# Performance work log

Measured on AMD Instinct MI355X. Metric: run time of the kernel, lower is better.

The kernel has to match this reference:

```python
import jax, jax.numpy as jnp
import numpy as np

D_MODEL = 1024
H = 16
D_K = D_MODEL // H  # 64
B, S = 2, 2048


def setup_inputs() -> dict:
    key = jax.random.key(0)
    ks = jax.random.split(key, 8)
    scale = 1.0 / np.sqrt(D_MODEL)
    return {
        "q": jax.random.normal(ks[0], (B, S, D_MODEL), dtype=jnp.float32),
        "k": jax.random.normal(ks[1], (B, S, D_MODEL), dtype=jnp.float32),
        "v": jax.random.normal(ks[2], (B, S, D_MODEL), dtype=jnp.float32),
        "W_q": jax.random.normal(ks[3], (H, D_MODEL, D_K), dtype=jnp.float32) * scale,
        "W_k": jax.random.normal(ks[4], (H, D_MODEL, D_K), dtype=jnp.float32) * scale,
        "W_v": jax.random.normal(ks[5], (H, D_MODEL, D_K), dtype=jnp.float32) * scale,
        "W_o": jax.random.normal(ks[6], (D_MODEL, H * D_K), dtype=jnp.float32) * scale,
        "b_o": jnp.zeros((D_MODEL,), dtype=jnp.float32),
    }


def reference(q, k, v, W_q, W_k, W_v, W_o, b_o):
    b, s, _ = q.shape
    h, _, d_k = W_q.shape
    inv_sqrt_dk = jnp.asarray(1.0 / np.sqrt(d_k), q.dtype)
    # per-head projections: [b, h, s, d_k]
    qh = jnp.einsum("bsd,hdk->bhsk", q, W_q)
    kh = jnp.einsum("bsd,hdk->bhsk", k, W_k)
    vh = jnp.einsum("bsd,hdk->bhsk", v, W_v)
    # scaled dot product attention
    scores = jnp.einsum("bhqk,bhsk->bhqs", qh, kh) * inv_sqrt_dk  # [b,h,S,S]
    attn = jax.nn.softmax(scores, axis=-1)
    ctx = jnp.einsum("bhqs,bhsk->bhqk", attn, vh)  # [b,h,S,d_k]
    # chunk over heads + concat along feature dim -> [b, S, h*d_k], head-major
    ctx = ctx.transpose(0, 2, 1, 3).reshape(b, s, h * d_k)
    # final linear
    return ctx @ W_o.T + b_o
```

## Files before the change

### kernel.cpp

```cpp
#include <hip/hip_runtime.h>
#include <cstdint>
#include <cstddef>


typedef unsigned short bf16_t;
typedef __attribute__((ext_vector_type(8))) short short8;
typedef __attribute__((ext_vector_type(4))) float f32x4;

__device__ __forceinline__ uint32_t fbits(float f) {
  union { float f; uint32_t u; } v; v.f = f; return v.u;
}
__device__ __forceinline__ bf16_t f2bf(float f) {
  uint32_t u = fbits(f);
  return (bf16_t)((u + 0x7FFFu + ((u >> 16) & 1u)) >> 16);
}
__device__ __forceinline__ uint32_t packbf2(float lo, float hi) {
  uint32_t a = fbits(hi) + 0x8000u;
  uint32_t b = fbits(lo) + 0x8000u;
  return __builtin_amdgcn_perm(a, b, 0x07060302u);
}
__device__ __forceinline__ int4 cvt8(f32x4 lo, f32x4 hi) {
  return make_int4((int)packbf2(lo.x, lo.y), (int)packbf2(lo.z, lo.w),
                   (int)packbf2(hi.x, hi.y), (int)packbf2(hi.z, hi.w));
}

__device__ __forceinline__ void gload16(const bf16_t* g, bf16_t* l) {
  __builtin_amdgcn_global_load_lds(
      (const __attribute__((address_space(1))) void*)g,
      (__attribute__((address_space(3))) void*)l, 16, 0, 0);
}

__global__ void prep_kernel(const float* __restrict__ Wo,
                            const float* __restrict__ Wq, const float* __restrict__ Wk,
                            const float* __restrict__ Wv,
                            const float* __restrict__ q, const float* __restrict__ k,
                            const float* __restrict__ v,
                            bf16_t* __restrict__ Woo,
                            bf16_t* __restrict__ Wtq, bf16_t* __restrict__ Wtk,
                            bf16_t* __restrict__ Wtv,
                            bf16_t* __restrict__ qb, bf16_t* __restrict__ kb,
                            bf16_t* __restrict__ vb) {
  int blk = blockIdx.x;
  int tid = threadIdx.x;
  if (blk < 1024) {
    int i = blk * 256 + tid;
    f32x4 val = ((const f32x4*)Wo)[i];
    ushort4 o;
    o.x = f2bf(val.x); o.y = f2bf(val.y); o.z = f2bf(val.z); o.w = f2bf(val.w);
    ((ushort4*)Woo)[i] = o;
  } else if (blk < 2560) {
    int blk2 = blk - 1024;
    int z = blk2 >> 9, t = blk2 & 511;
    const float* W = z == 0 ? Wq : z == 1 ? Wk : Wv;
    bf16_t* Wt = z == 0 ? Wtq : z == 1 ? Wtk : Wtv;
    int h = t >> 5, d0 = (t & 31) * 32;
    __shared__ float tile[32][65];
    const float* src = W + ((size_t)h << 16) + (size_t)d0 * 64;
    int d = tid >> 3;
#pragma unroll
    for (int j = 0; j < 2; j++) {
      int dk = (tid & 7) * 8 + j * 4;
      *(f32x4*)&tile[d][dk] = *(const f32x4*)(src + d * 64 + dk);
    }
    __syncthreads();
    int dk2 = tid >> 2, c = tid & 3;
    union { ushort s[8]; int4 v; } o;
#pragma unroll
    for (int j = 0; j < 8; j++) o.s[j] = f2bf(tile[c * 8 + j][dk2]);
    *(int4*)(Wt + (size_t)(h * 64 + dk2) * 1024 + d0 + c * 8) = o.v;
  } else {
    int blk3 = blk - 2560;
    int z = blk3 >> 11;
    int t3 = blk3 & 2047;
    const float* src = z == 0 ? q : z == 1 ? k : v;
    bf16_t* dst = z == 0 ? qb : z == 1 ? kb : vb;
    int i = t3 * 256 + tid;
    f32x4 lo = ((const f32x4*)src)[i * 2];
    f32x4 hi = ((const f32x4*)src)[i * 2 + 1];
    ((int4*)dst)[i] = cvt8(lo, hi);
  }
}

__global__ __launch_bounds__(256) void gemm_proj_kernel(
    const bf16_t* __restrict__ A0, const bf16_t* __restrict__ A1, const bf16_t* __restrict__ A2,
    const bf16_t* __restrict__ B0, const bf16_t* __restrict__ B1, const bf16_t* __restrict__ B2,
    bf16_t* __restrict__ O0, bf16_t* __restrict__ O1, bf16_t* __restrict__ O2,
    float s0)
{
  const int bid = blockIdx.x;
  const int nIdx = bid / 96;
  const int g = bid - nIdx * 96;
  const int z = g % 3;
  const int m0 = (g / 3) * 128, n0 = nIdx * 128;

  const bf16_t* A  = z == 0 ? A0 : z == 1 ? A1 : A2;
  const bf16_t* Bt = z == 0 ? B0 : z == 1 ? B1 : B2;
  bf16_t* Cout     = z == 0 ? O0 : z == 1 ? O1 : O2;
  const float scale = z == 0 ? s0 : 1.0f;
  const int K = 1024;

  __shared__ alignas(16) bf16_t smem[18432];

  const int tid = threadIdx.x;
  const int lane = tid & 63, wave = tid >> 6;
  const int wm = wave >> 1, wn = wave & 1;
  const int quad = lane >> 4, l15 = lane & 15;

  f32x4 acc[4][4];
#pragma unroll
  for (int i = 0; i < 4; i++)
#pragma unroll
    for (int j = 0; j < 4; j++) acc[i][j] = (f32x4)0.0f;

  const int srow = tid >> 2, scol = (tid & 3) * 8;
  const bf16_t* pa0 = A  + (size_t)(m0 + srow) * K + scol;
  const bf16_t* pa1 = pa0 + (size_t)64 * K;
  const bf16_t* pb0 = Bt + (size_t)(n0 + srow) * K + scol;
  const bf16_t* pb1 = pb0 + (size_t)64 * K;
  const int lws = wave * 512;

  gload16(pa0, smem + lws);
  gload16(pa1, smem + 2048 + lws);
  gload16(pb0, smem + 4096 + lws);
  gload16(pb1, smem + 6144 + lws);
  __syncthreads();

  for (int it = 0; it < 32; ++it) {
    const int cur = (it & 1) * 8192;
    if (it < 31) {
      const int nxt = ((it + 1) & 1) * 8192;
      const int ko = (it + 1) * 32;
      gload16(pa0 + ko, smem + nxt + lws);
      gload16(pa1 + ko, smem + nxt + 2048 + lws);
      gload16(pb0 + ko, smem + nxt + 4096 + lws);
      gload16(pb1 + ko, smem + nxt + 6144 + lws);
    }

    short8 af[4], bfr[4];
#pragma unroll
    for (int mi = 0; mi < 4; mi++)
      af[mi] = *(const short8*)(smem + cur + (wm * 64 + mi * 16 + l15) * 32 + quad * 8);
#pragma unroll
    for (int ni = 0; ni < 4; ni++)
      bfr[ni] = *(const short8*)(smem + cur + 4096 + (wn * 64 + ni * 16 + l15) * 32 + quad * 8);
#pragma unroll
    for (int mi = 0; mi < 4; mi++)
#pragma unroll
      for (int ni = 0; ni < 4; ni++)
        acc[mi][ni] = __builtin_amdgcn_mfma_f32_16x16x32_bf16(af[mi], bfr[ni], acc[mi][ni], 0, 0, 0);

    __syncthreads();
  }

  const int s0r = m0 & 2047, bb = m0 >> 11, hp = n0 >> 6;
  if (z < 2) {
    bf16_t* slot = smem + wn * 9216;
#pragma unroll
    for (int ni = 0; ni < 4; ni++)
#pragma unroll
      for (int mi = 0; mi < 4; mi++)
#pragma unroll
        for (int r = 0; r < 4; r++)
          slot[(wm * 64 + mi * 16 + quad * 4 + r) * 72 + ni * 16 + l15] =
              f2bf(acc[mi][ni][r] * scale);
    __syncthreads();
#pragma unroll
    for (int rd = 0; rd < 8; ++rd) {
      int idx = rd * 256 + tid;
      int si = idx >> 10, mm = (idx >> 3) & 127, c8 = idx & 7;
      int4 val = *(const int4*)(smem + si * 9216 + mm * 72 + c8 * 8);
      *(int4*)(Cout + ((size_t)((bb * 16 + hp + si) * 2048 + s0r + mm)) * 64 + c8 * 8) = val;
    }
  } else {
    bf16_t* slot = smem + wn * 8704;
#pragma unroll
    for (int ni = 0; ni < 4; ni++)
#pragma unroll
      for (int mi = 0; mi < 4; mi++) {
        uint2 pk = make_uint2(packbf2(acc[mi][ni][0], acc[mi][ni][1]),
                              packbf2(acc[mi][ni][2], acc[mi][ni][3]));
        *(uint2*)(slot + (ni * 16 + l15) * 136 + wm * 64 + mi * 16 + quad * 4) = pk;
      }
    __syncthreads();
#pragma unroll
    for (int rd = 0; rd < 8; ++rd) {
      int idx = rd * 256 + tid;
      int si = idx >> 10, c = (idx >> 4) & 63, ck = idx & 15;
      int4 val = *(const int4*)(smem + si * 8704 + c * 136 + ck * 8);
      *(int4*)(Cout + (size_t)(bb * 16 + hp + si) * 131072 + (size_t)c * 2048 + s0r + ck * 8) = val;
    }
  }
}

__global__ __launch_bounds__(256) void gemm_out_kernel(
    const bf16_t* __restrict__ A, const bf16_t* __restrict__ Bt,
    float* __restrict__ C, const float* __restrict__ bias)
{
  const int K = 1024, N = 1024;
  __shared__ alignas(16) bf16_t smem[12288];
  const int tid = threadIdx.x;
  const int lane = tid & 63, wave = tid >> 6;
  const int quad = lane >> 4, l15 = lane & 15;
  const int m0 = (blockIdx.x & 31) * 128, n0 = (blockIdx.x >> 5) * 64;

  f32x4 acc[2][4];
#pragma unroll
  for (int i = 0; i < 2; i++)
#pragma unroll
    for (int j = 0; j < 4; j++) acc[i][j] = (f32x4)0.0f;

  const int srow = tid >> 2, scol = (tid & 3) * 8;
  const bf16_t* pa0 = A  + (size_t)(m0 + srow) * K + scol;
  const bf16_t* pa1 = pa0 + (size_t)64 * K;
  const bf16_t* pb  = Bt + (size_t)(n0 + srow) * K + scol;
  const int lws = wave * 512;

  gload16(pa0, smem + lws);
  gload16(pa1, smem + 2048 + lws);
  gload16(pb,  smem + 4096 + lws);
  __syncthreads();

  for (int it = 0; it < 32; ++it) {
    const int cur = (it & 1) * 6144;
    if (it < 31) {
      const int nxt = ((it + 1) & 1) * 6144;
      const int ko = (it + 1) * 32;
      gload16(pa0 + ko, smem + nxt + lws);
      gload16(pa1 + ko, smem + nxt + 2048 + lws);
      gload16(pb + ko,  smem + nxt + 4096 + lws);
    }

    short8 af[2], bfr[4];
#pragma unroll
    for (int mi = 0; mi < 2; mi++)
      af[mi] = *(const short8*)(smem + cur + (wave * 32 + mi * 16 + l15) * 32 + quad * 8);
#pragma unroll
    for (int ni = 0; ni < 4; ni++)
      bfr[ni] = *(const short8*)(smem + cur + 4096 + (ni * 16 + l15) * 32 + quad * 8);
#pragma unroll
    for (int mi = 0; mi < 2; mi++)
#pragma unroll
      for (int ni = 0; ni < 4; ni++)
        acc[mi][ni] = __builtin_amdgcn_mfma_f32_16x16x32_bf16(af[mi], bfr[ni], acc[mi][ni], 0, 0, 0);

    __syncthreads();
  }

#pragma unroll
  for (int ni = 0; ni < 4; ni++) {
    int col = n0 + ni * 16 + l15;
    float bv = bias[col];
#pragma unroll
    for (int mi = 0; mi < 2; mi++) {
      int row = m0 + wave * 32 + mi * 16 + quad * 4;
#pragma unroll
      for (int r = 0; r < 4; r++)
        C[(size_t)(row + r) * N + col] = acc[mi][ni][r] + bv;
    }
  }
}

__global__ __launch_bounds__(256) void flash_kernel(
    const bf16_t* __restrict__ qh, const bf16_t* __restrict__ kh,
    const bf16_t* __restrict__ vT, bf16_t* __restrict__ ctx)
{
  __shared__ alignas(16) bf16_t KtF[2][4096];
  __shared__ alignas(16) bf16_t VtF[2][4096];
  __shared__ alignas(16) bf16_t PtF[8192];
  const int tid = threadIdx.x, lane = tid & 63, wave = tid >> 6;
  const int quad = lane >> 4, l15 = lane & 15;
  const int gid = blockIdx.x;
  const int hb = gid & 31;
  const int h = hb & 15, b = hb >> 4;
  const int q0 = (gid >> 5) * 128;
  const size_t headoff = (size_t)hb * 2048 * 64;
  const bf16_t* Q = qh + headoff;
  const bf16_t* K = kh + headoff;
  const bf16_t* V = vT + headoff;

  short8 qf[2][2];
#pragma unroll
  for (int g = 0; g < 2; g++)
#pragma unroll
    for (int ks = 0; ks < 2; ks++)
      qf[g][ks] = *(const short8*)(Q + (size_t)(q0 + wave * 32 + g * 16 + l15) * 64
                                   + ks * 32 + quad * 8);

  f32x4 O[2][4];
#pragma unroll
  for (int g = 0; g < 2; g++)
#pragma unroll
    for (int mi = 0; mi < 4; mi++) O[g][mi] = (f32x4)0.0f;
  f32x4 lacc[2] = {(f32x4)0.0f, (f32x4)0.0f};

  const bf16_t* Kp = K + (size_t)((wave >> 1) * 16 + l15) * 64 + (wave & 1) * 32 + quad * 8;
  const bf16_t* Vp = V + (size_t)((wave >> 1) * 16 + l15) * 2048 + (wave & 1) * 32 + quad * 8;
  const int lws = wave * 512;
  const int pwb = wave * 4096 + ((quad >> 1) * 16 + l15) * 16 + 8 * (quad & 1);

  auto stage = [&](int buf, int t) {
    gload16(Kp + (size_t)t * 4096,        &KtF[buf][lws]);
    gload16(Kp + (size_t)t * 4096 + 2048, &KtF[buf][lws + 2048]);
    gload16(Vp + (size_t)t * 64,          &VtF[buf][lws]);
    gload16(Vp + (size_t)t * 64 + 65536,  &VtF[buf][lws + 2048]);
  };

  auto body = [&](int buf) {
    f32x4 S[2][4];
#pragma unroll
    for (int g = 0; g < 2; g++)
#pragma unroll
      for (int mi = 0; mi < 4; mi++) S[g][mi] = (f32x4)0.0f;
    __builtin_amdgcn_s_setprio(1);
#pragma unroll
    for (int ks = 0; ks < 2; ks++) {
#pragma unroll
      for (int mi = 0; mi < 4; mi++) {
        short8 kf = *(const short8*)(&KtF[buf][(mi * 2 + ks) * 512 + lane * 8]);
        S[0][mi] = __builtin_amdgcn_mfma_f32_16x16x32_bf16(kf, qf[0][ks], S[0][mi], 0, 0, 0);
        S[1][mi] = __builtin_amdgcn_mfma_f32_16x16x32_bf16(kf, qf[1][ks], S[1][mi], 0, 0, 0);
      }
    }
    __builtin_amdgcn_s_setprio(0);
#pragma unroll
    for (int g = 0; g < 2; g++) {
#pragma unroll
      for (int mi = 0; mi < 4; mi++)
#pragma unroll
        for (int r = 0; r < 4; r++)
          S[g][mi][r] = __builtin_amdgcn_exp2f(S[g][mi][r]);
      lacc[g] += (S[g][0] + S[g][1]) + (S[g][2] + S[g][3]);
    }
#pragma unroll
    for (int g = 0; g < 2; g++)
#pragma unroll
      for (int mi = 0; mi < 4; mi++) {
        uint2 pk = make_uint2(packbf2(S[g][mi][0], S[g][mi][1]),
                              packbf2(S[g][mi][2], S[g][mi][3]));
        *(uint2*)((char*)PtF + pwb + g * 2048 + (mi >> 1) * 1024 + (mi & 1) * 512) = pk;
      }
    __builtin_amdgcn_s_setprio(1);
#pragma unroll
    for (int ks = 0; ks < 2; ks++) {
      short8 pf0 = *(const short8*)(&PtF[wave * 2048 + (ks * 64 + lane) * 8]);
      short8 pf1 = *(const short8*)(&PtF[wave * 2048 + 1024 + (ks * 64 + lane) * 8]);
#pragma unroll
      for (int mi = 0; mi < 4; mi++) {
        short8 vf = *(const short8*)(&VtF[buf][(mi * 2 + ks) * 512 + lane * 8]);
        O[0][mi] = __builtin_amdgcn_mfma_f32_16x16x32_bf16(vf, pf0, O[0][mi], 0, 0, 0);
        O[1][mi] = __builtin_amdgcn_mfma_f32_16x16x32_bf16(vf, pf1, O[1][mi], 0, 0, 0);
      }
    }
    __builtin_amdgcn_s_setprio(0);
  };

  stage(0, 0);
  __syncthreads();
  for (int it = 0; it < 32; ++it) {
    if (it < 31) stage((it + 1) & 1, it + 1);
    body(it & 1);
    __syncthreads();
  }

#pragma unroll
  for (int g = 0; g < 2; g++) {
    float l = (lacc[g][0] + lacc[g][1]) + (lacc[g][2] + lacc[g][3]);
    l += __shfl_xor(l, 16, 64);
    l += __shfl_xor(l, 32, 64);
    float inv = 1.0f / l;
    int qrow = q0 + wave * 32 + g * 16 + l15;
    bf16_t* crow = ctx + ((size_t)(b * 2048 + qrow)) * 1024 + h * 64;
#pragma unroll
    for (int mi = 0; mi < 4; mi++) {
      uint2 pk = make_uint2(packbf2(O[g][mi][0] * inv, O[g][mi][1] * inv),
                            packbf2(O[g][mi][2] * inv, O[g][mi][3] * inv));
      *(uint2*)(crow + mi * 16 + quad * 4) = pk;
    }
  }
}

extern "C" void kernel_launch(void* const* d_in, const int* in_sizes, int n_in,
                              void* d_out, int out_size, void* d_ws, size_t ws_size,
                              hipStream_t stream)
{
  const float* q  = (const float*)d_in[0];
  const float* k  = (const float*)d_in[1];
  const float* v  = (const float*)d_in[2];
  const float* Wq = (const float*)d_in[3];
  const float* Wk = (const float*)d_in[4];
  const float* Wv = (const float*)d_in[5];
  const float* Wo = (const float*)d_in[6];
  const float* bo = (const float*)d_in[7];
  float* out = (float*)d_out;

  const size_t NX = (size_t)4096 * 1024;
  const size_t NW = (size_t)1024 * 1024;

  char* p = (char*)d_ws;
  bf16_t* Wtq = (bf16_t*)p; p += NW * 2;
  bf16_t* Wtk = (bf16_t*)p; p += NW * 2;
  bf16_t* Wtv = (bf16_t*)p; p += NW * 2;
  bf16_t* Wob = (bf16_t*)p; p += NW * 2;
  bf16_t* qb  = (bf16_t*)p; p += NX * 2;
  bf16_t* kb  = (bf16_t*)p; p += NX * 2;
  bf16_t* vb  = (bf16_t*)p; p += NX * 2;
  bf16_t* qhb = (bf16_t*)p; p += NX * 2;
  bf16_t* khb = (bf16_t*)p; p += NX * 2;
  bf16_t* vTb = (bf16_t*)p; p += NX * 2;
  bf16_t* ctxb = (bf16_t*)p; p += NX * 2;

  prep_kernel<<<8704, 256, 0, stream>>>(Wo, Wq, Wk, Wv, q, k, v,
                                        Wob, Wtq, Wtk, Wtv, qb, kb, vb);

  const float qscale = 0.125f * 1.44269504088896340736f;
  gemm_proj_kernel<<<768, 256, 0, stream>>>(qb, kb, vb, Wtq, Wtk, Wtv,
                                            qhb, khb, vTb, qscale);

  flash_kernel<<<512, 256, 0, stream>>>(qhb, khb, vTb, ctxb);

  gemm_out_kernel<<<512, 256, 0, stream>>>(ctxb, Wob, out, bo);

  (void)in_sizes; (void)n_in; (void)out_size; (void)ws_size;
}
```

Measured before the change: 217.6 us.

## Use 512-thread flash blocks with register-staged K/V double buffering

Doubles the flash-attention block to 8 waves covering 256 query rows, so each K/V tile staged in shared memory is reused by twice as many queries and the grid halves. It replaces the direct global-to-LDS async loads with register-prefetched loads that are written to LDS one step ahead in an unrolled ping-pong loop, and removes the setprio hints. This trades fewer blocks and higher register pressure for K/V reuse, and the register path adds VGPR traffic that may reduce overlap.

```diff
diff --git a/kernel.cpp b/kernel.cpp
--- a/kernel.cpp
+++ b/kernel.cpp
@@ -260,19 +260,19 @@
   }
 }
 
-__global__ __launch_bounds__(256) void flash_kernel(
+__global__ __launch_bounds__(512) void flash_kernel(
     const bf16_t* __restrict__ qh, const bf16_t* __restrict__ kh,
     const bf16_t* __restrict__ vT, bf16_t* __restrict__ ctx)
 {
   __shared__ alignas(16) bf16_t KtF[2][4096];
   __shared__ alignas(16) bf16_t VtF[2][4096];
-  __shared__ alignas(16) bf16_t PtF[8192];
+  __shared__ alignas(16) bf16_t PtF[16384];
   const int tid = threadIdx.x, lane = tid & 63, wave = tid >> 6;
   const int quad = lane >> 4, l15 = lane & 15;
   const int gid = blockIdx.x;
   const int hb = gid & 31;
   const int h = hb & 15, b = hb >> 4;
-  const int q0 = (gid >> 5) * 128;
+  const int q0 = (gid >> 5) * 256;
   const size_t headoff = (size_t)hb * 2048 * 64;
   const bf16_t* Q = qh + headoff;
   const bf16_t* K = kh + headoff;
@@ -295,15 +295,8 @@
 
   const bf16_t* Kp = K + (size_t)((wave >> 1) * 16 + l15) * 64 + (wave & 1) * 32 + quad * 8;
   const bf16_t* Vp = V + (size_t)((wave >> 1) * 16 + l15) * 2048 + (wave & 1) * 32 + quad * 8;
-  const int lws = wave * 512;
+  const int soff = wave * 512 + lane * 8;
   const int pwb = wave * 4096 + ((quad >> 1) * 16 + l15) * 16 + 8 * (quad & 1);
-
-  auto stage = [&](int buf, int t) {
-    gload16(Kp + (size_t)t * 4096,        &KtF[buf][lws]);
-    gload16(Kp + (size_t)t * 4096 + 2048, &KtF[buf][lws + 2048]);
-    gload16(Vp + (size_t)t * 64,          &VtF[buf][lws]);
-    gload16(Vp + (size_t)t * 64 + 65536,  &VtF[buf][lws + 2048]);
-  };
 
   auto body = [&](int buf) {
     f32x4 S[2][4];
@@ -311,7 +304,6 @@
     for (int g = 0; g < 2; g++)
 #pragma unroll
       for (int mi = 0; mi < 4; mi++) S[g][mi] = (f32x4)0.0f;
-    __builtin_amdgcn_s_setprio(1);
 #pragma unroll
     for (int ks = 0; ks < 2; ks++) {
 #pragma unroll
@@ -321,7 +313,6 @@
         S[1][mi] = __builtin_amdgcn_mfma_f32_16x16x32_bf16(kf, qf[1][ks], S[1][mi], 0, 0, 0);
       }
     }
-    __builtin_amdgcn_s_setprio(0);
 #pragma unroll
     for (int g = 0; g < 2; g++) {
 #pragma unroll
@@ -339,7 +330,6 @@
                               packbf2(S[g][mi][2], S[g][mi][3]));
         *(uint2*)((char*)PtF + pwb + g * 2048 + (mi >> 1) * 1024 + (mi & 1) * 512) = pk;
       }
-    __builtin_amdgcn_s_setprio(1);
 #pragma unroll
     for (int ks = 0; ks < 2; ks++) {
       short8 pf0 = *(const short8*)(&PtF[wave * 2048 + (ks * 64 + lane) * 8]);
@@ -351,14 +341,34 @@
         O[1][mi] = __builtin_amdgcn_mfma_f32_16x16x32_bf16(vf, pf1, O[1][mi], 0, 0, 0);
       }
     }
-    __builtin_amdgcn_s_setprio(0);
   };
 
-  stage(0, 0);
+  int4 k0 = *(const int4*)Kp, v0 = *(const int4*)Vp;
+  *(int4*)(&KtF[0][soff]) = k0;
+  *(int4*)(&VtF[0][soff]) = v0;
+  int4 kA = *(const int4*)(Kp + 4096), vA = *(const int4*)(Vp + 64);
   __syncthreads();
-  for (int it = 0; it < 32; ++it) {
-    if (it < 31) stage((it + 1) & 1, it + 1);
-    body(it & 1);
+
+  for (int it = 0; it < 32; it += 2) {
+    *(int4*)(&KtF[1][soff]) = kA;
+    *(int4*)(&VtF[1][soff]) = vA;
+    int4 kB, vB;
+    if (it + 2 < 32) {
+      kB = *(const int4*)(Kp + (size_t)(it + 2) * 4096);
+      vB = *(const int4*)(Vp + (size_t)(it + 2) * 64);
+    }
+    body(0);
+    __syncthreads();
+
+    if (it + 2 < 32) {
+      *(int4*)(&KtF[0][soff]) = kB;
+      *(int4*)(&VtF[0][soff]) = vB;
+    }
+    if (it + 3 < 32) {
+      kA = *(const int4*)(Kp + (size_t)(it + 3) * 4096);
+      vA = *(const int4*)(Vp + (size_t)(it + 3) * 64);
+    }
+    body(1);
     __syncthreads();
   }
 
@@ -416,7 +426,7 @@
   gemm_proj_kernel<<<768, 256, 0, stream>>>(qb, kb, vb, Wtq, Wtk, Wtv,
                                             qhb, khb, vTb, qscale);
 
-  flash_kernel<<<512, 256, 0, stream>>>(qhb, khb, vTb, ctxb);
+  flash_kernel<<<256, 512, 0, stream>>>(qhb, khb, vTb, ctxb);
 
   gemm_out_kernel<<<512, 256, 0, stream>>>(ctxb, Wob, out, bo);
 
```

Measured after the change: 208.8 us. 4.0% less time.
